# Optimization experiments

Hardware: AMD Instinct MI355X
Metric: run time of the kernel (lower is better)

## Reference

```python
import jax, jax.numpy as jnp
import numpy as np

N_NODES = 50000
N_EDGES = 300000
EMB = 256
HID = 512
L = 5
BN_EPS = 1e-5


def setup_inputs() -> dict:
    key = jax.random.key(0)
    ks = jax.random.split(key, 12)
    return {
        "node_ids": jax.random.randint(ks[0], (N_NODES,), 0, 100),
        "node_depth": jax.random.randint(ks[1], (N_NODES,), 0, 20),
        "edge_index": jax.random.randint(ks[2], (2, N_EDGES), 0, N_NODES),
        "edge_attr": jax.random.normal(ks[3], (N_EDGES, 2), jnp.float32),
        "node_type_emb": jax.random.normal(ks[4], (100, EMB), jnp.float32) * 0.1,
        "depth_emb": jax.random.normal(ks[5], (21, EMB), jnp.float32) * 0.1,
        "We": jax.random.normal(ks[6], (L, 2, EMB), jnp.float32) * 0.1,
        "be": jnp.zeros((L, EMB), jnp.float32),
        "W1": jax.random.normal(ks[7], (L, EMB, HID), jnp.float32) * (1.0 / np.sqrt(EMB)),
        "b1": jnp.zeros((L, HID), jnp.float32),
        "gamma": jnp.ones((L, HID), jnp.float32),
        "beta": jnp.zeros((L, HID), jnp.float32),
        "W2": jax.random.normal(ks[8], (L, HID, EMB), jnp.float32) * (1.0 / np.sqrt(HID)),
        "b2": jnp.zeros((L, EMB), jnp.float32),
        "eps_param": jnp.zeros((L,), jnp.float32),
    }


def reference(node_ids, node_depth, edge_index, edge_attr, node_type_emb,
              depth_emb, We, be, W1, b1, gamma, beta, W2, b2, eps_param):
    n = node_ids.shape[0]
    src, dst = edge_index[0], edge_index[1]
    # node encoder (code task): type embedding + clipped depth embedding
    depth = jnp.clip(node_depth, 0, depth_emb.shape[0] - 1)
    h = node_type_emb[node_ids] + depth_emb[depth]  # [N, EMB]
    n_layers = We.shape[0]
    for l in range(n_layers):
        e = edge_attr @ We[l] + be[l]  # [E, EMB] edge encoding
        msg = jax.nn.relu(h[src] + e)  # gather + relu
        agg = jax.ops.segment_sum(msg, dst, num_segments=n)  # scatter-add
        z = (1.0 + eps_param[l]) * h + agg
        # MLP: Linear -> BatchNorm1d (batch stats) -> ReLU -> Linear
        y = z @ W1[l] + b1[l]  # [N, HID]
        mu = jnp.mean(y, axis=0)
        var = jnp.var(y, axis=0)
        y = (y - mu) * jax.lax.rsqrt(var + BN_EPS) * gamma[l] + beta[l]
        y = jax.nn.relu(y)
        h_new = y @ W2[l] + b2[l]  # [N, EMB]
        if l < n_layers - 1:
            h_new = jax.nn.relu(h_new)  # dropout is identity (drop_ratio=0)
        h = h_new
    return h
```

## Files before the change

### kernel.cpp

```cpp
#include <hip/hip_runtime.h>

#define NN 50000
#define NE 300000
#define EMB 256
#define HID 512
#define NL 5

typedef __attribute__((ext_vector_type(8))) short bf16x8;
typedef __attribute__((ext_vector_type(4))) float f32x4;
typedef __attribute__((ext_vector_type(8))) unsigned short u16x8;
typedef __attribute__((ext_vector_type(4))) unsigned short u16x4;

union U8u { u16x8 v; bf16x8 b; unsigned short s[8]; };

__device__ __forceinline__ float bf2f(unsigned short u) {
  union { unsigned int i; float f; } c; c.i = ((unsigned int)u) << 16; return c.f;
}
__device__ __forceinline__ unsigned short f2bf(float f) {
  union { float f; unsigned int i; } c; c.f = f;
  unsigned int r = c.i + 0x7FFF + ((c.i >> 16) & 1);
  return (unsigned short)(r >> 16);
}

__global__ __launch_bounds__(256) void k_init_h(const int* __restrict__ ids,
    const int* __restrict__ depth, const float* __restrict__ temb,
    const float* __restrict__ demb, float* __restrict__ h) {
  int gid = blockIdx.x * 256 + threadIdx.x;
  int row = gid >> 6;
  if (row >= NN) return;
  int c4 = (gid & 63) << 2;
  int id = ids[row];
  int d = depth[row]; d = d < 0 ? 0 : (d > 20 ? 20 : d);
  float4 a = *(const float4*)&temb[id * EMB + c4];
  float4 b = *(const float4*)&demb[d * EMB + c4];
  *(float4*)&h[row * EMB + c4] = make_float4(a.x + b.x, a.y + b.y, a.z + b.z, a.w + b.w);
}

__global__ __launch_bounds__(256) void k_count(const int* __restrict__ dst, int* __restrict__ deg) {
  int e = blockIdx.x * 256 + threadIdx.x;
  if (e < NE) atomicAdd(&deg[dst[e]], 1);
}
__global__ __launch_bounds__(256) void k_scan1(const int* __restrict__ deg,
    int* __restrict__ row_off, int* __restrict__ bsums) {
  __shared__ int lds[256];
  int b = blockIdx.x, t = threadIdx.x;
  int base = b * 1024;
  int v[4]; int s = 0;
  for (int i = 0; i < 4; ++i) {
    int idx = base + t * 4 + i;
    v[i] = (idx < NN) ? deg[idx] : 0;
    s += v[i];
  }
  lds[t] = s; __syncthreads();
  for (int off = 1; off < 256; off <<= 1) {
    int x = (t >= off) ? lds[t - off] : 0; __syncthreads();
    lds[t] += x; __syncthreads();
  }
  int run = (t > 0) ? lds[t - 1] : 0;
  if (t == 255) bsums[b] = lds[255];
  for (int i = 0; i < 4; ++i) {
    int idx = base + t * 4 + i;
    if (idx < NN) row_off[idx] = run;
    run += v[i];
  }
}
__global__ __launch_bounds__(256) void k_scan2(int* __restrict__ bsums, int nb) {
  __shared__ int lds[256];
  int t = threadIdx.x;
  int v = (t < nb) ? bsums[t] : 0;
  lds[t] = v; __syncthreads();
  for (int off = 1; off < 256; off <<= 1) {
    int x = (t >= off) ? lds[t - off] : 0; __syncthreads();
    lds[t] += x; __syncthreads();
  }
  if (t < nb) bsums[t] = (t > 0) ? lds[t - 1] : 0;
}
__global__ __launch_bounds__(256) void k_scan3(int* __restrict__ row_off, const int* __restrict__ bsums) {
  int b = blockIdx.x, t = threadIdx.x;
  int base = b * 1024;
  int add = bsums[b];
  for (int i = 0; i < 4; ++i) {
    int idx = base + t * 4 + i;
    if (idx < NN) row_off[idx] += add;
  }
  if (b == 0 && t == 0) row_off[NN] = NE;
}
__global__ __launch_bounds__(256) void k_copy(const int* __restrict__ a, int* __restrict__ b) {
  int i = blockIdx.x * 256 + threadIdx.x;
  if (i < NN) b[i] = a[i];
}
__global__ __launch_bounds__(256) void k_fill(const int* __restrict__ src, const int* __restrict__ dst,
    const float* __restrict__ attr, int* __restrict__ cursor,
    int* __restrict__ ssrc, float2* __restrict__ sattr) {
  int e = blockIdx.x * 256 + threadIdx.x;
  if (e >= NE) return;
  int d = dst[e];
  int p = atomicAdd(&cursor[d], 1);
  ssrc[p] = src[e];
  sattr[p] = make_float2(attr[2 * e], attr[2 * e + 1]);
}

__global__ __launch_bounds__(256) void k_convW(const float* __restrict__ W,
    unsigned short* __restrict__ Wt, int R, int C) {
  __shared__ float t[32][33];
  int l = blockIdx.z;
  const float* Wl = W + (size_t)l * R * C;
  unsigned short* Wtl = Wt + (size_t)l * R * C;
  int c0 = blockIdx.x * 32, r0 = blockIdx.y * 32;
  int tx = threadIdx.x & 31, ty = threadIdx.x >> 5;
  for (int i = 0; i < 32; i += 8)
    t[ty + i][tx] = Wl[(size_t)(r0 + ty + i) * C + c0 + tx];
  __syncthreads();
  for (int i = 0; i < 32; i += 8)
    Wtl[(size_t)(c0 + ty + i) * R + r0 + tx] = f2bf(t[tx][ty + i]);
}

__global__ __launch_bounds__(256) void k_aggregate(const float* __restrict__ h,
    const int* __restrict__ row_off, const int* __restrict__ ssrc,
    const float2* __restrict__ sattr, const float* __restrict__ We_l,
    const float* __restrict__ be_l, const float* __restrict__ epsp, int layer,
    unsigned short* __restrict__ z) {
  int wid = (blockIdx.x * 256 + threadIdx.x) >> 6;
  if (wid >= NN) return;
  int c4 = (threadIdx.x & 63) << 2;
  float4 w0 = *(const float4*)&We_l[c4];
  float4 w1 = *(const float4*)&We_l[EMB + c4];
  float4 bb = *(const float4*)&be_l[c4];
  float4 acc = make_float4(0.f, 0.f, 0.f, 0.f);
  int k0 = row_off[wid], k1 = row_off[wid + 1];
  for (int k = k0; k < k1; ++k) {
    int s = ssrc[k];
    float2 a = sattr[k];
    float4 hv = *(const float4*)&h[(size_t)s * EMB + c4];
    acc.x += fmaxf(hv.x + a.x * w0.x + a.y * w1.x + bb.x, 0.f);
    acc.y += fmaxf(hv.y + a.x * w0.y + a.y * w1.y + bb.y, 0.f);
    acc.z += fmaxf(hv.z + a.x * w0.z + a.y * w1.z + bb.z, 0.f);
    acc.w += fmaxf(hv.w + a.x * w0.w + a.y * w1.w + bb.w, 0.f);
  }
  float e1 = 1.0f + epsp[layer];
  float4 hv = *(const float4*)&h[(size_t)wid * EMB + c4];
  u16x4 o;
  o[0] = f2bf(e1 * hv.x + acc.x);
  o[1] = f2bf(e1 * hv.y + acc.y);
  o[2] = f2bf(e1 * hv.z + acc.z);
  o[3] = f2bf(e1 * hv.w + acc.w);
  *(u16x4*)&z[(size_t)wid * EMB + c4] = o;
}

template<int K, int NC, int MODE>
__global__ __launch_bounds__(256) void k_gemm(
    const unsigned short* __restrict__ A, const unsigned short* __restrict__ Bt,
    const float* __restrict__ bias, const float* __restrict__ scale,
    const float* __restrict__ shift, unsigned short* __restrict__ Ybf,
    float* __restrict__ Hout, float* __restrict__ colsum, float* __restrict__ colsq) {
  constexpr int KT = K / 32;
  __shared__ __align__(16) unsigned short lA[2][128 * 32];
  __shared__ __align__(16) unsigned short lB[2][128 * 32];
  const int tid = threadIdx.x;
  const int lane = tid & 63, wave = tid >> 6;
  const int lr = lane & 15, lg = lane >> 4;
  const int wr = (wave >> 1) * 64, wc = (wave & 1) * 64;
  const int col0 = blockIdx.x * 128, row0 = blockIdx.y * 128;

  const int rA = tid >> 1;
  const int hA = (tid & 1) * 16;
  int grs = row0 + rA; if (grs > NN - 1) grs = NN - 1;
  const unsigned short* aSrc = A + (size_t)grs * K + hA;
  const unsigned short* bSrc = Bt + (size_t)(col0 + rA) * K + hA;
  unsigned short* aDst = &lA[0][0] + rA * 32 + hA;
  unsigned short* bDst = &lB[0][0] + rA * 32 + hA;

  f32x4 acc[4][4] = {};
  u16x8 ra0, ra1, rb0, rb1;
  f32x4 sc[4], sh[4];

  auto tload = [&](int kt) {
    ra0 = *(const u16x8*)(aSrc + kt * 32);
    ra1 = *(const u16x8*)(aSrc + kt * 32 + 8);
    rb0 = *(const u16x8*)(bSrc + kt * 32);
    rb1 = *(const u16x8*)(bSrc + kt * 32 + 8);
    if constexpr (MODE >= 1) {
      int kb = kt * 32 + hA;
#pragma unroll
      for (int q = 0; q < 4; ++q) {
        sc[q] = *(const f32x4*)&scale[kb + q * 4];
        sh[q] = *(const f32x4*)&shift[kb + q * 4];
      }
    }
  };
  auto twrite = [&](int buf) {
    u16x8 wa0 = ra0, wa1 = ra1;
    if constexpr (MODE >= 1) {
      U8u a0, a1, o0, o1;
      a0.v = ra0; a1.v = ra1;
#pragma unroll
      for (int j = 0; j < 4; ++j) {
        o0.s[j]     = f2bf(fmaxf(bf2f(a0.s[j])     * sc[0][j] + sh[0][j], 0.f));
        o0.s[4 + j] = f2bf(fmaxf(bf2f(a0.s[4 + j]) * sc[1][j] + sh[1][j], 0.f));
        o1.s[j]     = f2bf(fmaxf(bf2f(a1.s[j])     * sc[2][j] + sh[2][j], 0.f));
        o1.s[4 + j] = f2bf(fmaxf(bf2f(a1.s[4 + j]) * sc[3][j] + sh[3][j], 0.f));
      }
      wa0 = o0.v; wa1 = o1.v;
    }
    *(u16x8*)(aDst + buf * 4096) = wa0;
    *(u16x8*)(aDst + buf * 4096 + 8) = wa1;
    *(u16x8*)(bDst + buf * 4096) = rb0;
    *(u16x8*)(bDst + buf * 4096 + 8) = rb1;
  };

  tload(0); twrite(0);
  __syncthreads();
  int buf = 0;
  for (int kt = 0; kt < KT; ++kt) {
    if (kt + 1 < KT) tload(kt + 1);
    bf16x8 af[4], bfr[4];
#pragma unroll
    for (int m = 0; m < 4; ++m)
      af[m] = *(const bf16x8*)&lA[buf][(wr + m * 16 + lr) * 32 + lg * 8];
#pragma unroll
    for (int n = 0; n < 4; ++n)
      bfr[n] = *(const bf16x8*)&lB[buf][(wc + n * 16 + lr) * 32 + lg * 8];
#pragma unroll
    for (int m = 0; m < 4; ++m)
#pragma unroll
      for (int n = 0; n < 4; ++n)
        acc[m][n] = __builtin_amdgcn_mfma_f32_16x16x32_bf16(bfr[n], af[m], acc[m][n], 0, 0, 0);
    if (kt + 1 < KT) twrite(buf ^ 1);
    __syncthreads();
    buf ^= 1;
  }

  if constexpr (MODE == 0) {
    f32x4 csum[4] = {}, csq[4] = {};
#pragma unroll
    for (int n = 0; n < 4; ++n) {
      const int gcB = col0 + wc + n * 16 + lg * 4;
      f32x4 bv = *(const f32x4*)&bias[gcB];
#pragma unroll
      for (int m = 0; m < 4; ++m) {
        int gr = row0 + wr + m * 16 + lr;
        if (gr < NN) {
          f32x4 v = acc[m][n] + bv;
          u16x4 o;
#pragma unroll
          for (int j = 0; j < 4; ++j) o[j] = f2bf(v[j]);
          *(u16x4*)&Ybf[(size_t)gr * NC + gcB] = o;
          csum[n] += v;
          csq[n] += v * v;
        }
      }
    }
#pragma unroll
    for (int n = 0; n < 4; ++n)
#pragma unroll
      for (int j = 0; j < 4; ++j) {
        float s = csum[n][j], q = csq[n][j];
        s += __shfl_xor(s, 1, 64); q += __shfl_xor(q, 1, 64);
        s += __shfl_xor(s, 2, 64); q += __shfl_xor(q, 2, 64);
        s += __shfl_xor(s, 4, 64); q += __shfl_xor(q, 4, 64);
        s += __shfl_xor(s, 8, 64); q += __shfl_xor(q, 8, 64);
        if (lr == 0) {
          atomicAdd(&colsum[col0 + wc + n * 16 + lg * 4 + j], s);
          atomicAdd(&colsq[col0 + wc + n * 16 + lg * 4 + j], q);
        }
      }
  } else {
#pragma unroll
    for (int n = 0; n < 4; ++n) {
      const int gcB = col0 + wc + n * 16 + lg * 4;
      f32x4 bv = *(const f32x4*)&bias[gcB];
#pragma unroll
      for (int m = 0; m < 4; ++m) {
        int gr = row0 + wr + m * 16 + lr;
        if (gr < NN) {
          f32x4 v = acc[m][n] + bv;
          if constexpr (MODE == 1) {
#pragma unroll
            for (int j = 0; j < 4; ++j) v[j] = fmaxf(v[j], 0.f);
          }
          *(f32x4*)&Hout[(size_t)gr * NC + gcB] = v;
        }
      }
    }
  }
}

__global__ void k_bnfin(const float* __restrict__ colsum, const float* __restrict__ colsq,
    const float* __restrict__ gamma, const float* __restrict__ beta,
    float* __restrict__ scale, float* __restrict__ shift) {
  int c = threadIdx.x;
  float inv_n = 1.0f / (float)NN;
  float mu = colsum[c] * inv_n;
  float var = colsq[c] * inv_n - mu * mu;
  float rstd = rsqrtf(var + 1e-5f);
  float sc = rstd * gamma[c];
  scale[c] = sc;
  shift[c] = beta[c] - mu * sc;
}

extern "C" void kernel_launch(void* const* d_in, const int* in_sizes, int n_in,
                              void* d_out, int out_size, void* d_ws, size_t ws_size,
                              hipStream_t stream) {
  (void)in_sizes; (void)n_in; (void)out_size; (void)ws_size;
  const int* node_ids    = (const int*)d_in[0];
  const int* node_depth  = (const int*)d_in[1];
  const int* edge_index  = (const int*)d_in[2];
  const float* edge_attr = (const float*)d_in[3];
  const float* temb      = (const float*)d_in[4];
  const float* demb      = (const float*)d_in[5];
  const float* We        = (const float*)d_in[6];
  const float* be        = (const float*)d_in[7];
  const float* W1        = (const float*)d_in[8];
  const float* b1        = (const float*)d_in[9];
  const float* gamma_    = (const float*)d_in[10];
  const float* beta_     = (const float*)d_in[11];
  const float* W2        = (const float*)d_in[12];
  const float* b2        = (const float*)d_in[13];
  const float* epsp      = (const float*)d_in[14];
  float* h = (float*)d_out;

  char* ws = (char*)d_ws;
  size_t off = 0;
  auto alloc = [&](size_t bytes) -> void* {
    void* p = ws + off;
    off = (off + bytes + 255) & ~(size_t)255;
    return p;
  };
  unsigned short* z   = (unsigned short*)alloc(2ull * NN * EMB);
  unsigned short* y   = (unsigned short*)alloc(2ull * NN * HID);
  unsigned short* W1t = (unsigned short*)alloc(2ull * NL * EMB * HID);
  unsigned short* W2t = (unsigned short*)alloc(2ull * NL * HID * EMB);
  int* deg      = (int*)alloc(sizeof(int) * NN);
  int* row_off  = (int*)alloc(sizeof(int) * (NN + 1));
  int* cursor   = (int*)alloc(sizeof(int) * NN);
  int* ssrc     = (int*)alloc(sizeof(int) * NE);
  float2* sattr = (float2*)alloc(sizeof(float2) * NE);
  int* bsums    = (int*)alloc(sizeof(int) * 256);
  float* colsum = (float*)alloc(sizeof(float) * HID * 2);
  float* colsq  = colsum + HID;
  float* scale  = (float*)alloc(sizeof(float) * HID);
  float* shift  = (float*)alloc(sizeof(float) * HID);

  const int* e_src = edge_index;
  const int* e_dst = edge_index + NE;

  k_init_h<<<(NN * 64) / 256, 256, 0, stream>>>(node_ids, node_depth, temb, demb, h);
  hipMemsetAsync(deg, 0, sizeof(int) * NN, stream);
  k_count<<<(NE + 255) / 256, 256, 0, stream>>>(e_dst, deg);
  k_scan1<<<49, 256, 0, stream>>>(deg, row_off, bsums);
  k_scan2<<<1, 256, 0, stream>>>(bsums, 49);
  k_scan3<<<49, 256, 0, stream>>>(row_off, bsums);
  k_copy<<<(NN + 255) / 256, 256, 0, stream>>>(row_off, cursor);
  k_fill<<<(NE + 255) / 256, 256, 0, stream>>>(e_src, e_dst, edge_attr, cursor, ssrc, sattr);
  k_convW<<<dim3(HID / 32, EMB / 32, NL), 256, 0, stream>>>(W1, W1t, EMB, HID);
  k_convW<<<dim3(EMB / 32, HID / 32, NL), 256, 0, stream>>>(W2, W2t, HID, EMB);

  const int MB = (NN + 127) / 128;
  for (int l = 0; l < NL; ++l) {
    k_aggregate<<<(NN * 64) / 256, 256, 0, stream>>>(
        h, row_off, ssrc, sattr, We + (size_t)l * 2 * EMB, be + (size_t)l * EMB, epsp, l, z);
    hipMemsetAsync(colsum, 0, sizeof(float) * HID * 2, stream);
    k_gemm<EMB, HID, 0><<<dim3(HID / 128, MB), 256, 0, stream>>>(
        z, W1t + (size_t)l * EMB * HID, b1 + (size_t)l * HID,
        nullptr, nullptr, y, nullptr, colsum, colsq);
    k_bnfin<<<1, HID, 0, stream>>>(colsum, colsq, gamma_ + (size_t)l * HID,
                                   beta_ + (size_t)l * HID, scale, shift);
    if (l < NL - 1)
      k_gemm<HID, EMB, 1><<<dim3(EMB / 128, MB), 256, 0, stream>>>(
          y, W2t + (size_t)l * HID * EMB, b2 + (size_t)l * EMB,
          scale, shift, nullptr, h, nullptr, nullptr);
    else
      k_gemm<HID, EMB, 2><<<dim3(EMB / 128, MB), 256, 0, stream>>>(
          y, W2t + (size_t)l * HID * EMB, b2 + (size_t)l * EMB,
          scale, shift, nullptr, h, nullptr, nullptr);
  }
}
```

Before: 1.250 ms.

## Stage GEMM tiles via direct global-to-LDS loads and split out BN apply

The GEMM now copies A and B tiles straight from global memory into LDS using global_load_lds, instead of going through registers. This removes the register round-trip and frees VGPRs. Because the BatchNorm scale/shift/ReLU can no longer be fused into that staging step, it moves into a separate elementwise pass over y, which costs an extra read and write of the hidden activations. The launch grid is also flattened with a grouped block remap so that blocks sharing row tiles run close together, for better L2 reuse.

After: 1.222 ms. 1.02x faster.

```diff
diff --git a/kernel.cpp b/kernel.cpp
--- a/kernel.cpp
+++ b/kernel.cpp
@@ -20,6 +20,11 @@
   union { float f; unsigned int i; } c; c.f = f;
   unsigned int r = c.i + 0x7FFF + ((c.i >> 16) & 1);
   return (unsigned short)(r >> 16);
+}
+__device__ __forceinline__ void gload_lds16(const void* g, void* l) {
+  __builtin_amdgcn_global_load_lds(
+      (const __attribute__((address_space(1))) void*)g,
+      (__attribute__((address_space(3))) void*)l, 16, 0, 0);
 }
 
 __global__ __launch_bounds__(256) void k_init_h(const int* __restrict__ ids,
@@ -150,69 +155,50 @@
 template<int K, int NC, int MODE>
 __global__ __launch_bounds__(256) void k_gemm(
     const unsigned short* __restrict__ A, const unsigned short* __restrict__ Bt,
-    const float* __restrict__ bias, const float* __restrict__ scale,
-    const float* __restrict__ shift, unsigned short* __restrict__ Ybf,
+    const float* __restrict__ bias, unsigned short* __restrict__ Ybf,
     float* __restrict__ Hout, float* __restrict__ colsum, float* __restrict__ colsq) {
   constexpr int KT = K / 32;
+  constexpr int NCB = NC / 128;
   __shared__ __align__(16) unsigned short lA[2][128 * 32];
   __shared__ __align__(16) unsigned short lB[2][128 * 32];
+
+  int b = blockIdx.x;
+  int q = b >> 3;
+  int colb = q % NCB;
+  int rowb = (b & 7) + 8 * (q / NCB);
+  if (rowb * 128 >= NN) return;
+  const int row0 = rowb * 128, col0 = colb * 128;
+
   const int tid = threadIdx.x;
   const int lane = tid & 63, wave = tid >> 6;
   const int lr = lane & 15, lg = lane >> 4;
   const int wr = (wave >> 1) * 64, wc = (wave & 1) * 64;
-  const int col0 = blockIdx.x * 128, row0 = blockIdx.y * 128;
-
-  const int rA = tid >> 1;
-  const int hA = (tid & 1) * 16;
-  int grs = row0 + rA; if (grs > NN - 1) grs = NN - 1;
-  const unsigned short* aSrc = A + (size_t)grs * K + hA;
-  const unsigned short* bSrc = Bt + (size_t)(col0 + rA) * K + hA;
-  unsigned short* aDst = &lA[0][0] + rA * 32 + hA;
-  unsigned short* bDst = &lB[0][0] + rA * 32 + hA;
+
+  int aR0 = row0 + wave * 32 + (lane >> 2);
+  int aR1 = aR0 + 16;
+  if (aR0 > NN - 1) aR0 = NN - 1;
+  if (aR1 > NN - 1) aR1 = NN - 1;
+  const int kc = (lane & 3) * 8;
+  const unsigned short* aS0 = A + (size_t)aR0 * K + kc;
+  const unsigned short* aS1 = A + (size_t)aR1 * K + kc;
+  const unsigned short* bS0 = Bt + (size_t)(col0 + wave * 32 + (lane >> 2)) * K + kc;
+  const unsigned short* bS1 = bS0 + (size_t)16 * K;
 
   f32x4 acc[4][4] = {};
-  u16x8 ra0, ra1, rb0, rb1;
-  f32x4 sc[4], sh[4];
-
-  auto tload = [&](int kt) {
-    ra0 = *(const u16x8*)(aSrc + kt * 32);
-    ra1 = *(const u16x8*)(aSrc + kt * 32 + 8);
-    rb0 = *(const u16x8*)(bSrc + kt * 32);
-    rb1 = *(const u16x8*)(bSrc + kt * 32 + 8);
-    if constexpr (MODE >= 1) {
-      int kb = kt * 32 + hA;
-#pragma unroll
-      for (int q = 0; q < 4; ++q) {
-        sc[q] = *(const f32x4*)&scale[kb + q * 4];
-        sh[q] = *(const f32x4*)&shift[kb + q * 4];
-      }
-    }
+
+  auto stage = [&](int buf, int kt) {
+    int ko = kt * 32;
+    gload_lds16(aS0 + ko, &lA[buf][wave * 1024]);
+    gload_lds16(aS1 + ko, &lA[buf][wave * 1024 + 512]);
+    gload_lds16(bS0 + ko, &lB[buf][wave * 1024]);
+    gload_lds16(bS1 + ko, &lB[buf][wave * 1024 + 512]);
   };
-  auto twrite = [&](int buf) {
-    u16x8 wa0 = ra0, wa1 = ra1;
-    if constexpr (MODE >= 1) {
-      U8u a0, a1, o0, o1;
-      a0.v = ra0; a1.v = ra1;
-#pragma unroll
-      for (int j = 0; j < 4; ++j) {
-        o0.s[j]     = f2bf(fmaxf(bf2f(a0.s[j])     * sc[0][j] + sh[0][j], 0.f));
-        o0.s[4 + j] = f2bf(fmaxf(bf2f(a0.s[4 + j]) * sc[1][j] + sh[1][j], 0.f));
-        o1.s[j]     = f2bf(fmaxf(bf2f(a1.s[j])     * sc[2][j] + sh[2][j], 0.f));
-        o1.s[4 + j] = f2bf(fmaxf(bf2f(a1.s[4 + j]) * sc[3][j] + sh[3][j], 0.f));
-      }
-      wa0 = o0.v; wa1 = o1.v;
-    }
-    *(u16x8*)(aDst + buf * 4096) = wa0;
-    *(u16x8*)(aDst + buf * 4096 + 8) = wa1;
-    *(u16x8*)(bDst + buf * 4096) = rb0;
-    *(u16x8*)(bDst + buf * 4096 + 8) = rb1;
-  };
-
-  tload(0); twrite(0);
+
+  stage(0, 0);
   __syncthreads();
   int buf = 0;
   for (int kt = 0; kt < KT; ++kt) {
-    if (kt + 1 < KT) tload(kt + 1);
+    if (kt + 1 < KT) stage(buf ^ 1, kt + 1);
     bf16x8 af[4], bfr[4];
 #pragma unroll
     for (int m = 0; m < 4; ++m)
@@ -225,7 +211,6 @@
 #pragma unroll
       for (int n = 0; n < 4; ++n)
         acc[m][n] = __builtin_amdgcn_mfma_f32_16x16x32_bf16(bfr[n], af[m], acc[m][n], 0, 0, 0);
-    if (kt + 1 < KT) twrite(buf ^ 1);
     __syncthreads();
     buf ^= 1;
   }
@@ -254,14 +239,14 @@
     for (int n = 0; n < 4; ++n)
 #pragma unroll
       for (int j = 0; j < 4; ++j) {
-        float s = csum[n][j], q = csq[n][j];
-        s += __shfl_xor(s, 1, 64); q += __shfl_xor(q, 1, 64);
-        s += __shfl_xor(s, 2, 64); q += __shfl_xor(q, 2, 64);
-        s += __shfl_xor(s, 4, 64); q += __shfl_xor(q, 4, 64);
-        s += __shfl_xor(s, 8, 64); q += __shfl_xor(q, 8, 64);
+        float s = csum[n][j], qq = csq[n][j];
+        s += __shfl_xor(s, 1, 64); qq += __shfl_xor(qq, 1, 64);
+        s += __shfl_xor(s, 2, 64); qq += __shfl_xor(qq, 2, 64);
+        s += __shfl_xor(s, 4, 64); qq += __shfl_xor(qq, 4, 64);
+        s += __shfl_xor(s, 8, 64); qq += __shfl_xor(qq, 8, 64);
         if (lr == 0) {
           atomicAdd(&colsum[col0 + wc + n * 16 + lg * 4 + j], s);
-          atomicAdd(&colsq[col0 + wc + n * 16 + lg * 4 + j], q);
+          atomicAdd(&colsq[col0 + wc + n * 16 + lg * 4 + j], qq);
         }
       }
   } else {
@@ -296,6 +281,24 @@
   float sc = rstd * gamma[c];
   scale[c] = sc;
   shift[c] = beta[c] - mu * sc;
+}
+
+__global__ __launch_bounds__(256) void k_bnapply(unsigned short* __restrict__ y,
+    const float* __restrict__ scale, const float* __restrict__ shift) {
+  const int total = NN * (HID / 8);
+  for (int idx = blockIdx.x * 256 + threadIdx.x; idx < total; idx += gridDim.x * 256) {
+    int c8 = (idx & (HID / 8 - 1)) * 8;
+    U8u a; a.v = *(const u16x8*)&y[(size_t)idx * 8];
+    f32x4 s0 = *(const f32x4*)&scale[c8], s1 = *(const f32x4*)&scale[c8 + 4];
+    f32x4 t0 = *(const f32x4*)&shift[c8], t1 = *(const f32x4*)&shift[c8 + 4];
+    U8u o;
+#pragma unroll
+    for (int j = 0; j < 4; ++j) {
+      o.s[j]     = f2bf(fmaxf(bf2f(a.s[j])     * s0[j] + t0[j], 0.f));
+      o.s[4 + j] = f2bf(fmaxf(bf2f(a.s[4 + j]) * s1[j] + t1[j], 0.f));
+    }
+    *(u16x8*)&y[(size_t)idx * 8] = o.v;
+  }
 }
 
 extern "C" void kernel_launch(void* const* d_in, const int* in_sizes, int n_in,
@@ -356,22 +359,23 @@
   k_convW<<<dim3(EMB / 32, HID / 32, NL), 256, 0, stream>>>(W2, W2t, HID, EMB);
 
   const int MB = (NN + 127) / 128;
+  const int RG8 = (MB + 7) / 8;
+  const int G1 = 8 * (HID / 128) * RG8;
+  const int G2 = 8 * (EMB / 128) * RG8;
   for (int l = 0; l < NL; ++l) {
     k_aggregate<<<(NN * 64) / 256, 256, 0, stream>>>(
         h, row_off, ssrc, sattr, We + (size_t)l * 2 * EMB, be + (size_t)l * EMB, epsp, l, z);
     hipMemsetAsync(colsum, 0, sizeof(float) * HID * 2, stream);
-    k_gemm<EMB, HID, 0><<<dim3(HID / 128, MB), 256, 0, stream>>>(
-        z, W1t + (size_t)l * EMB * HID, b1 + (size_t)l * HID,
-        nullptr, nullptr, y, nullptr, colsum, colsq);
+    k_gemm<EMB, HID, 0><<<G1, 256, 0, stream>>>(
+        z, W1t + (size_t)l * EMB * HID, b1 + (size_t)l * HID, y, nullptr, colsum, colsq);
     k_bnfin<<<1, HID, 0, stream>>>(colsum, colsq, gamma_ + (size_t)l * HID,
                                    beta_ + (size_t)l * HID, scale, shift);
+    k_bnapply<<<2048, 256, 0, stream>>>(y, scale, shift);
     if (l < NL - 1)
-      k_gemm<HID, EMB, 1><<<dim3(EMB / 128, MB), 256, 0, stream>>>(
-          y, W2t + (size_t)l * HID * EMB, b2 + (size_t)l * EMB,
-          scale, shift, nullptr, h, nullptr, nullptr);
+      k_gemm<HID, EMB, 1><<<G2, 256, 0, stream>>>(
+          y, W2t + (size_t)l * HID * EMB, b2 + (size_t)l * EMB, nullptr, h, nullptr, nullptr);
     else
-      k_gemm<HID, EMB, 2><<<dim3(EMB / 128, MB), 256, 0, stream>>>(
-          y, W2t + (size_t)l * HID * EMB, b2 + (size_t)l * EMB,
-          scale, shift, nullptr, h, nullptr, nullptr);
-  }
-}
+      k_gemm<HID, EMB, 2><<<G2, 256, 0, stream>>>(
+          y, W2t + (size_t)l * HID * EMB, b2 + (size_t)l * EMB, nullptr, h, nullptr, nullptr);
+  }
+}
```
